# Kernel tuning notes

Measured on AMD Instinct MI355X. Metric: run time of the kernel, lower is better.

The kernel has to match this reference:

```python
import jax, jax.numpy as jnp
import numpy as np

N_NODES = 55
N_FEAT = 48
BATCH = 16384


def _norm_adj():
    # tridiagonal adjacency with self-loops, row-normalized by degree
    i = jnp.arange(N_NODES)
    A = (jnp.abs(i[:, None] - i[None, :]) <= 1).astype(jnp.float32)  # [55,55]
    return A / A.sum(axis=1, keepdims=True)  # D^{-1} A


def setup_inputs() -> dict:
    key = jax.random.key(0)
    k1, k2, k3 = jax.random.split(key, 3)
    x = jax.random.normal(k1, (BATCH, N_NODES, N_FEAT), dtype=jnp.float32)
    W = jax.random.normal(k2, (N_FEAT, N_FEAT), dtype=jnp.float32) * (1.0 / np.sqrt(N_FEAT))
    b = jax.random.normal(k3, (N_FEAT,), dtype=jnp.float32) * 0.01
    return {"x": x, "W": W, "b": b}


def reference(x, W, b):
    DA = _norm_adj()                                  # [55,55]
    AX = jnp.einsum('ij,bjf->bif', DA, x)             # banded neighbor avg
    # nn.Linear: y = AX @ W^T + b, then ReLU
    return jax.nn.relu(jnp.einsum('bif,of->bio', AX, W) + b)
```

## Files before the change

kernel.cpp:

```cpp
#include <hip/hip_runtime.h>


#define NODES 55
#define F 48
#define BT 4
#define NP 56
#define ROWS (BT * NP)
#define ST 72

typedef __attribute__((ext_vector_type(8))) short short8_t;
typedef __attribute__((ext_vector_type(4))) float floatx4;

__device__ __forceinline__ unsigned short f2bf(float f) {
    union { float f; unsigned int u; } v; v.f = f;
    unsigned int u = v.u;
    u += 0x7FFFu + ((u >> 16) & 1u);
    return (unsigned short)(u >> 16);
}

__global__ __launch_bounds__(256, 4)
void gconv_kernel(const float* __restrict__ x, const float* __restrict__ W,
                  const float* __restrict__ bias, float* __restrict__ out) {
    __shared__ unsigned short s_ax[ROWS * ST];
    __shared__ unsigned short s_w[F * ST];

    const int tid = threadIdx.x;
    const int b0 = blockIdx.x * BT;

    for (int i = tid; i < 220 * 4; i += 256) {
        int r = i >> 2, c = i & 3;
        *(uint2*)&s_ax[r * ST + 48 + c * 4] = make_uint2(0u, 0u);
    }
    for (int i = tid; i < 4 * 18; i += 256) {
        int r = 220 + i / 18, c = i % 18;
        *(uint2*)&s_ax[r * ST + c * 4] = make_uint2(0u, 0u);
    }
    for (int i = tid; i < 48 * 4; i += 256) {
        int r = i >> 2, c = i & 3;
        *(uint2*)&s_w[r * ST + 48 + c * 4] = make_uint2(0u, 0u);
    }

    for (int i = tid; i < F * F; i += 256) {
        int o = i / 48, f = i - o * 48;
        s_w[o * ST + f] = f2bf(W[i]);
    }

    const float4* xg = reinterpret_cast<const float4*>(x);
    for (int task = tid; task < BT * NODES * 12; task += 256) {
        int b_l  = task / 660;
        int rem  = task - b_l * 660;
        int node = rem / 12;
        int fq   = rem - node * 12;
        int gidx = ((b0 + b_l) * NODES + node) * 12 + fq;
        float4 c = xg[gidx];
        float sx = c.x, sy = c.y, sz = c.z, sw = c.w;
        if (node > 0)  { float4 l = xg[gidx - 12]; sx += l.x; sy += l.y; sz += l.z; sw += l.w; }
        if (node < 54) { float4 r = xg[gidx + 12]; sx += r.x; sy += r.y; sz += r.z; sw += r.w; }
        float wgt = (node == 0 || node == 54) ? 0.5f : (1.0f / 3.0f);
        sx *= wgt; sy *= wgt; sz *= wgt; sw *= wgt;
        unsigned int lo = (unsigned int)f2bf(sx) | ((unsigned int)f2bf(sy) << 16);
        unsigned int hi = (unsigned int)f2bf(sz) | ((unsigned int)f2bf(sw) << 16);
        int r_ = node * BT + b_l;
        *(uint2*)&s_ax[r_ * ST + fq * 4] = make_uint2(lo, hi);
    }
    __syncthreads();

    const int lane = tid & 63;
    const int wave = tid >> 6;
    const int col  = lane & 15;
    const int quad = lane >> 4;

    short8_t wf[3][2];
#pragma unroll
    for (int nt = 0; nt < 3; ++nt)
#pragma unroll
        for (int s = 0; s < 2; ++s)
            wf[nt][s] = *(const short8_t*)&s_w[(nt * 16 + col) * ST + s * 32 + quad * 8];

    float bv[3];
#pragma unroll
    for (int nt = 0; nt < 3; ++nt) bv[nt] = bias[nt * 16 + col];

    for (int m = wave; m < 14; m += 4) {
        const int r_ = m * 16 + col;
        short8_t a0 = *(const short8_t*)&s_ax[r_ * ST + quad * 8];
        short8_t a1 = *(const short8_t*)&s_ax[r_ * ST + 32 + quad * 8];

        floatx4 acc0 = {0.f, 0.f, 0.f, 0.f};
        floatx4 acc1 = {0.f, 0.f, 0.f, 0.f};
        floatx4 acc2 = {0.f, 0.f, 0.f, 0.f};
        acc0 = __builtin_amdgcn_mfma_f32_16x16x32_bf16(a0, wf[0][0], acc0, 0, 0, 0);
        acc1 = __builtin_amdgcn_mfma_f32_16x16x32_bf16(a0, wf[1][0], acc1, 0, 0, 0);
        acc2 = __builtin_amdgcn_mfma_f32_16x16x32_bf16(a0, wf[2][0], acc2, 0, 0, 0);
        acc0 = __builtin_amdgcn_mfma_f32_16x16x32_bf16(a1, wf[0][1], acc0, 0, 0, 0);
        acc1 = __builtin_amdgcn_mfma_f32_16x16x32_bf16(a1, wf[1][1], acc1, 0, 0, 0);
        acc2 = __builtin_amdgcn_mfma_f32_16x16x32_bf16(a1, wf[2][1], acc2, 0, 0, 0);

#pragma unroll
        for (int j = 0; j < 4; ++j) {
            int r2   = m * 16 + quad * 4 + j;
            int node = r2 >> 2;
            int b_l  = r2 & 3;
            if (node < NODES) {
                int obase = ((b0 + b_l) * NODES + node) * F + col;
                float v0 = acc0[j] + bv[0]; v0 = v0 > 0.f ? v0 : 0.f;
                float v1 = acc1[j] + bv[1]; v1 = v1 > 0.f ? v1 : 0.f;
                float v2 = acc2[j] + bv[2]; v2 = v2 > 0.f ? v2 : 0.f;
                out[obase]      = v0;
                out[obase + 16] = v1;
                out[obase + 32] = v2;
            }
        }
    }
}

extern "C" void kernel_launch(void* const* d_in, const int* in_sizes, int n_in,
                              void* d_out, int out_size, void* d_ws, size_t ws_size,
                              hipStream_t stream) {
    const float* x    = (const float*)d_in[0];
    const float* W    = (const float*)d_in[1];
    const float* bias = (const float*)d_in[2];
    float* out = (float*)d_out;
    const int BATCH = 16384;
    dim3 grid(BATCH / BT);
    dim3 block(256);
    gconv_kernel<<<grid, block, 0, stream>>>(x, W, bias, out);
}
```

Before: 333.5 us.

## Reuse neighbor loads via sliding window and shrink LDS row padding

Each of 240 threads now loads a window of 13 consecutive nodes for one batch/feature quad and computes 11 averaged outputs from registers, replacing three global loads per output with about 13/11. The LDS row stride drops from 72 to 56 halfwords, and the K padding columns are replaced by zeroing the upper half of the second MFMA operand in registers. This removes most of the zero-fill loops and cuts LDS footprint, which may raise occupancy. The catch is that only 240 threads do the load phase and each holds 13 float4 values, which raises register pressure, and the new stride may change LDS bank-conflict behaviour.

```diff
diff --git a/kernel.cpp b/kernel.cpp
--- a/kernel.cpp
+++ b/kernel.cpp
@@ -4,9 +4,8 @@
 #define NODES 55
 #define F 48
 #define BT 4
-#define NP 56
-#define ROWS (BT * NP)
-#define ST 72
+#define ROWS 224
+#define ST 56
 
 typedef __attribute__((ext_vector_type(8))) short short8_t;
 typedef __attribute__((ext_vector_type(4))) float floatx4;
@@ -27,17 +26,12 @@
     const int tid = threadIdx.x;
     const int b0 = blockIdx.x * BT;
 
-    for (int i = tid; i < 220 * 4; i += 256) {
-        int r = i >> 2, c = i & 3;
-        *(uint2*)&s_ax[r * ST + 48 + c * 4] = make_uint2(0u, 0u);
-    }
-    for (int i = tid; i < 4 * 18; i += 256) {
-        int r = 220 + i / 18, c = i % 18;
-        *(uint2*)&s_ax[r * ST + c * 4] = make_uint2(0u, 0u);
-    }
-    for (int i = tid; i < 48 * 4; i += 256) {
-        int r = i >> 2, c = i & 3;
-        *(uint2*)&s_w[r * ST + 48 + c * 4] = make_uint2(0u, 0u);
+    if (tid >= 240) {
+        int i = tid - 240;
+        for (int t = i; t < 48; t += 16) {
+            int row = 220 + (t / 12), c = t - (t / 12) * 12;
+            *(uint2*)&s_ax[row * ST + c * 4] = make_uint2(0u, 0u);
+        }
     }
 
     for (int i = tid; i < F * F; i += 256) {
@@ -45,23 +39,40 @@
         s_w[o * ST + f] = f2bf(W[i]);
     }
 
-    const float4* xg = reinterpret_cast<const float4*>(x);
-    for (int task = tid; task < BT * NODES * 12; task += 256) {
-        int b_l  = task / 660;
-        int rem  = task - b_l * 660;
-        int node = rem / 12;
-        int fq   = rem - node * 12;
-        int gidx = ((b0 + b_l) * NODES + node) * 12 + fq;
-        float4 c = xg[gidx];
-        float sx = c.x, sy = c.y, sz = c.z, sw = c.w;
-        if (node > 0)  { float4 l = xg[gidx - 12]; sx += l.x; sy += l.y; sz += l.z; sw += l.w; }
-        if (node < 54) { float4 r = xg[gidx + 12]; sx += r.x; sy += r.y; sz += r.z; sw += r.w; }
-        float wgt = (node == 0 || node == 54) ? 0.5f : (1.0f / 3.0f);
-        sx *= wgt; sy *= wgt; sz *= wgt; sw *= wgt;
-        unsigned int lo = (unsigned int)f2bf(sx) | ((unsigned int)f2bf(sy) << 16);
-        unsigned int hi = (unsigned int)f2bf(sz) | ((unsigned int)f2bf(sw) << 16);
-        int r_ = node * BT + b_l;
-        *(uint2*)&s_ax[r_ * ST + fq * 4] = make_uint2(lo, hi);
+    if (tid < 240) {
+        const int s   = tid / 48;
+        const int rem = tid - s * 48;
+        const int b_l = rem / 12;
+        const int fq  = rem - b_l * 12;
+        const float4* xg = reinterpret_cast<const float4*>(x);
+        const int base = (b0 + b_l) * (NODES * 12) + fq;
+        const int n0 = s * 11;
+
+        float4 v[13];
+#pragma unroll
+        for (int t = 0; t < 13; ++t) {
+            int n = n0 - 1 + t;
+            int nc = n < 0 ? 0 : (n > 54 ? 54 : n);
+            float4 tmp = xg[base + nc * 12];
+            bool ok = (n >= 0) & (n <= 54);
+            v[t].x = ok ? tmp.x : 0.f;
+            v[t].y = ok ? tmp.y : 0.f;
+            v[t].z = ok ? tmp.z : 0.f;
+            v[t].w = ok ? tmp.w : 0.f;
+        }
+
+#pragma unroll
+        for (int t = 0; t < 11; ++t) {
+            int n = n0 + t;
+            float w = (n == 0 || n == 54) ? 0.5f : (1.0f / 3.0f);
+            float sx = (v[t].x + v[t + 1].x + v[t + 2].x) * w;
+            float sy = (v[t].y + v[t + 1].y + v[t + 2].y) * w;
+            float sz = (v[t].z + v[t + 1].z + v[t + 2].z) * w;
+            float sw = (v[t].w + v[t + 1].w + v[t + 2].w) * w;
+            unsigned int lo = (unsigned int)f2bf(sx) | ((unsigned int)f2bf(sy) << 16);
+            unsigned int hi = (unsigned int)f2bf(sz) | ((unsigned int)f2bf(sw) << 16);
+            *(uint2*)&s_ax[(n * BT + b_l) * ST + fq * 4] = make_uint2(lo, hi);
+        }
     }
     __syncthreads();
 
@@ -70,12 +81,15 @@
     const int col  = lane & 15;
     const int quad = lane >> 4;
 
+    const short8_t zero8 = {0, 0, 0, 0, 0, 0, 0, 0};
+
     short8_t wf[3][2];
 #pragma unroll
-    for (int nt = 0; nt < 3; ++nt)
-#pragma unroll
-        for (int s = 0; s < 2; ++s)
-            wf[nt][s] = *(const short8_t*)&s_w[(nt * 16 + col) * ST + s * 32 + quad * 8];
+    for (int nt = 0; nt < 3; ++nt) {
+        wf[nt][0] = *(const short8_t*)&s_w[(nt * 16 + col) * ST + quad * 8];
+        short8_t t1 = *(const short8_t*)&s_w[(nt * 16 + col) * ST + 32 + (quad & 1) * 8];
+        wf[nt][1] = (quad < 2) ? t1 : zero8;
+    }
 
     float bv[3];
 #pragma unroll
@@ -84,7 +98,8 @@
     for (int m = wave; m < 14; m += 4) {
         const int r_ = m * 16 + col;
         short8_t a0 = *(const short8_t*)&s_ax[r_ * ST + quad * 8];
-        short8_t a1 = *(const short8_t*)&s_ax[r_ * ST + 32 + quad * 8];
+        short8_t t1 = *(const short8_t*)&s_ax[r_ * ST + 32 + (quad & 1) * 8];
+        short8_t a1 = (quad < 2) ? t1 : zero8;
 
         floatx4 acc0 = {0.f, 0.f, 0.f, 0.f};
         floatx4 acc1 = {0.f, 0.f, 0.f, 0.f};
```

Measured after the change: 299.6 us. -10.2%, faster.
